# Kernel tuning notes

Hardware: AMD Instinct MI355X
Metric: run time of the kernel (lower is better)

## Reference

```python
import jax, jax.numpy as jnp
import numpy as np

# ---- hyperparameters (from init_kwargs) ----
B, SEQ, D_MODEL = 2, 2048, 1024
D_STATE, D_CONV, EXPAND, HEAD_DIM, CHUNK = 128, 4, 2, 64, 256
D_INNER = EXPAND * D_MODEL            # 2048
NH = D_INNER // HEAD_DIM              # 32 heads
CONV_DIM = D_INNER + 2 * D_STATE      # 2304
D_IN_PROJ = 2 * D_INNER + 2 * D_STATE + NH  # z, xBC, dt -> 4384
D_FF = 4 * D_MODEL
EPS = 1e-12


def setup_inputs() -> dict:
    key = jax.random.key(0)
    ks = jax.random.split(key, 16)
    s = 0.02
    f32 = jnp.float32
    inp = {
        "x": jax.random.normal(ks[0], (B, SEQ, D_MODEL), f32),
        "time_diff": jax.random.uniform(ks[1], (B, SEQ), f32),
        # TiSSD (Mamba2-style) params
        "W_in": jax.random.normal(ks[2], (D_MODEL, D_IN_PROJ), f32) * s,
        "b_in": jnp.zeros((D_IN_PROJ,), f32),
        "conv_w": jax.random.normal(ks[3], (CONV_DIM, D_CONV), f32) * s,
        "conv_b": jnp.zeros((CONV_DIM,), f32),
        "A_log": jnp.log(jnp.arange(1, NH + 1, dtype=f32)),
        "dt_bias": jnp.full((NH,), -2.0, f32),
        "D": jnp.ones((NH,), f32),
        "time_decay": jnp.full((NH,), -3.0, f32),   # time-aware decay rates
        "rms_w": jnp.ones((D_INNER,), f32),
        "W_out": jax.random.normal(ks[4], (D_INNER, D_MODEL), f32) * s,
        "b_out": jnp.zeros((D_MODEL,), f32),
        # wrapper LayerNorm
        "ln_g": jnp.ones((D_MODEL,), f32),
        "ln_b": jnp.zeros((D_MODEL,), f32),
        # FFN
        "fc1_w": jax.random.normal(ks[5], (D_MODEL, D_FF), f32) * s,
        "fc1_b": jnp.zeros((D_FF,), f32),
        "fc2_w": jax.random.normal(ks[6], (D_FF, D_MODEL), f32) * s,
        "fc2_b": jnp.zeros((D_MODEL,), f32),
        "ln2_g": jnp.ones((D_MODEL,), f32),
        "ln2_b": jnp.zeros((D_MODEL,), f32),
    }
    return inp


def _layer_norm(x, g, b, eps=EPS):
    mu = jnp.mean(x, axis=-1, keepdims=True)
    var = jnp.mean(jnp.square(x - mu), axis=-1, keepdims=True)
    return (x - mu) * jax.lax.rsqrt(var + eps) * g + b


def _hardswish(x):
    return x * jnp.clip(x + 3.0, 0.0, 6.0) * (1.0 / 6.0)


def _tissd_forward(x, time_diff, W_in, b_in, conv_w, conv_b, A_log, dt_bias, D,
                   time_decay, rms_w, W_out, b_out):
    b, l, _ = x.shape
    zxbcdt = x @ W_in + b_in                       # [b,l,D_IN_PROJ]
    z = zxbcdt[..., :D_INNER]
    xBC = zxbcdt[..., D_INNER:D_INNER + CONV_DIM]
    dt_raw = zxbcdt[..., -NH:]

    # causal depthwise conv1d (small fixed kernel -> unrolled shifts)
    xp = jnp.pad(xBC, ((0, 0), (D_CONV - 1, 0), (0, 0)))
    xBC_c = conv_b
    for k in range(D_CONV):
        xBC_c = xBC_c + xp[:, k:k + l, :] * conv_w[:, k]
    xBC_c = jax.nn.silu(xBC_c)

    xs = xBC_c[..., :D_INNER]
    Bm = xBC_c[..., D_INNER:D_INNER + D_STATE]     # [b,l,n]
    Cm = xBC_c[..., -D_STATE:]                     # [b,l,n]

    dt = jax.nn.softplus(dt_raw + dt_bias)         # [b,l,h]
    A = -jnp.exp(A_log)                            # [h]
    # time-aware: extra decay proportional to time gap
    dA = dt * A - jax.nn.softplus(time_decay) * time_diff[..., None]  # [b,l,h]

    xh = xs.reshape(b, l, NH, HEAD_DIM)
    xdt = xh * dt[..., None]                       # [b,l,h,p]

    nc = l // CHUNK
    xc = xdt.reshape(b, nc, CHUNK, NH, HEAD_DIM)
    Bc = Bm.reshape(b, nc, CHUNK, D_STATE)
    Cc = Cm.reshape(b, nc, CHUNK, D_STATE)
    dAc = dA.reshape(b, nc, CHUNK, NH).transpose(0, 3, 1, 2)  # [b,h,c,L]

    A_cum = jnp.cumsum(dAc, axis=-1)               # [b,h,c,L]
    seg = A_cum[..., :, None] - A_cum[..., None, :]
    mask = jnp.tril(jnp.ones((CHUNK, CHUNK), bool))
    Lmat = jnp.where(mask, jnp.exp(jnp.where(mask, seg, 0.0)), 0.0)  # [b,h,c,L,L]

    # intra-chunk (diagonal block) output
    Y_diag = jnp.einsum("bcln,bcsn,bhcls,bcshp->bclhp", Cc, Bc, Lmat, xc)

    # per-chunk final states
    decay_states = jnp.exp(A_cum[..., -1:] - A_cum)  # [b,h,c,L]
    states = jnp.einsum("bcln,bhcl,bclhp->bchpn", Bc, decay_states, xc)
    chunk_decay = jnp.exp(A_cum[..., -1])            # [b,h,c]

    # inter-chunk recurrence over nc chunks
    states_t = states.transpose(1, 0, 2, 3, 4)       # [c,b,h,p,n]
    decay_t = chunk_decay.transpose(2, 0, 1)         # [c,b,h]

    def step(carry, inp):
        s_c, d_c = inp
        new = carry * d_c[..., None, None] + s_c
        return new, carry                            # emit state BEFORE chunk

    init = jnp.zeros((b, NH, HEAD_DIM, D_STATE), x.dtype)
    _, prev_states = jax.lax.scan(step, init, (states_t, decay_t))
    prev_states = prev_states.transpose(1, 0, 2, 3, 4)  # [b,c,h,p,n]

    state_decay = jnp.exp(A_cum)                     # [b,h,c,L]
    Y_off = jnp.einsum("bcln,bchpn,bhcl->bclhp", Cc, prev_states, state_decay)

    Y = (Y_diag + Y_off).reshape(b, l, NH, HEAD_DIM) + D[None, None, :, None] * xh
    y = Y.reshape(b, l, D_INNER)

    # gated RMSNorm
    y = y * jax.nn.silu(z)
    y = y * jax.lax.rsqrt(jnp.mean(jnp.square(y), axis=-1, keepdims=True) + EPS) * rms_w
    return y @ W_out + b_out


def reference(x, time_diff, W_in, b_in, conv_w, conv_b, A_log, dt_bias, D,
              time_decay, rms_w, W_out, b_out, ln_g, ln_b,
              fc1_w, fc1_b, fc2_w, fc2_b, ln2_g, ln2_b):
    hidden = _tissd_forward(x, time_diff, W_in, b_in, conv_w, conv_b, A_log,
                            dt_bias, D, time_decay, rms_w, W_out, b_out)
    # num_layers > 1 -> residual; dropout is identity in eval mode
    h = _layer_norm(hidden + x, ln_g, ln_b)
    # FFN with Hardswish and residual LayerNorm
    hid = _hardswish(h @ fc1_w + fc1_b)
    hid = hid @ fc2_w + fc2_b
    out = _layer_norm(hid + h, ln2_g, ln2_b)
    return (out, time_diff)
```

## Files before the change

### kernel.cpp

```cpp
#include <hip/hip_runtime.h>

#define BATCH 2
#define SEQL 2048
#define DM 1024
#define DSTATE 128
#define HD 64
#define CHUNK 256
#define DI 2048
#define NHEADS 32
#define CONVD 2304
#define DPROJ 4384
#define DPROJ_PAD 4608
#define DFF 4096
#define NC 8
#define ROWS (BATCH*SEQL)

typedef unsigned short ushort_t;
typedef short bf16x8 __attribute__((ext_vector_type(8)));
typedef float f32x4 __attribute__((ext_vector_type(4)));

__device__ __forceinline__ float softplus_f(float v){
    return (v > 20.f) ? v : log1pf(expf(v));
}
__device__ __forceinline__ float silu_f(float v){
    return v / (1.f + expf(-v));
}
__device__ __forceinline__ ushort_t f2b(float v){
    union { float f; unsigned int u; } x; x.f = v;
    unsigned int r = x.u + 0x7fffu + ((x.u >> 16) & 1u);
    return (ushort_t)(r >> 16);
}
__device__ __forceinline__ float b2f(ushort_t v){
    union { unsigned int u; float f; } x; x.u = ((unsigned int)v) << 16;
    return x.f;
}

template<int ACT, int OUT_BF16, int TN, int NS, int DTX>
__global__ __launch_bounds__(256) void mfma_gemm_k(
    const ushort_t* __restrict__ A, const ushort_t* __restrict__ Bt,
    const float* __restrict__ bias, float* __restrict__ Cf,
    ushort_t* __restrict__ Cb, float* __restrict__ dtaux,
    int M, int N, int K, int ldc)
{
    constexpr int NT = (TN == 128) ? 4 : 2;
    constexpr int BROWS = TN / 4;
    __shared__ ushort_t As[128*64];
    __shared__ ushort_t Bs[TN*64];
    int tid = threadIdx.x;
    int lane = tid & 63, wave = tid >> 6;
    int m0 = blockIdx.y * 128, n0 = blockIdx.x * TN;
    int Ks = K / NS;
    int kb = (NS > 1) ? blockIdx.z * Ks : 0;
    int wave_m = (TN==128) ? (wave >> 1)*64 : (wave & 1)*64;
    int wave_n = (TN==128) ? (wave & 1)*64 : (wave >> 1)*32;
    int lrow = lane >> 3;
    int lcol = ((lane & 7) ^ lrow) * 8;
    const ushort_t* Abase = A  + (size_t)(m0 + wave*32    + lrow)*K + lcol + kb;
    const ushort_t* Bbase = Bt + (size_t)(n0 + wave*BROWS + lrow)*K + lcol + kb;
    ushort_t* AsW = &As[(wave*32)*64];
    ushort_t* BsW = &Bs[(wave*BROWS)*64];
    f32x4 acc[4][NT];
    #pragma unroll
    for (int i=0;i<4;i++)
        #pragma unroll
        for (int j=0;j<NT;j++) acc[i][j] = (f32x4){0.f,0.f,0.f,0.f};
    int lm = lane & 15;
    int quad = lane >> 4;
    for (int k0 = 0; k0 < Ks; k0 += 64){
        #pragma unroll
        for (int j = 0; j < 4; j++)
            __builtin_amdgcn_global_load_lds(
                (const __attribute__((address_space(1))) void*)(Abase + (size_t)(j*8)*K + k0),
                (__attribute__((address_space(3))) void*)(AsW + j*8*64), 16, 0, 0);
        #pragma unroll
        for (int j = 0; j < BROWS/8; j++)
            __builtin_amdgcn_global_load_lds(
                (const __attribute__((address_space(1))) void*)(Bbase + (size_t)(j*8)*K + k0),
                (__attribute__((address_space(3))) void*)(BsW + j*8*64), 16, 0, 0);
        __syncthreads();
        #pragma unroll
        for (int kk = 0; kk < 64; kk += 32){
            int cb = kk >> 3;
            bf16x8 af[4], bfr[NT];
            #pragma unroll
            for (int mt=0; mt<4; mt++)
                af[mt] = *(const bf16x8*)&As[(wave_m + mt*16 + lm)*64 + (((cb + quad) ^ (lm & 7))*8)];
            #pragma unroll
            for (int nt=0; nt<NT; nt++)
                bfr[nt] = *(const bf16x8*)&Bs[(wave_n + nt*16 + lm)*64 + (((cb + quad) ^ (lm & 7))*8)];
            #pragma unroll
            for (int mt=0; mt<4; mt++)
                #pragma unroll
                for (int nt=0; nt<NT; nt++)
                    acc[mt][nt] = __builtin_amdgcn_mfma_f32_16x16x32_bf16(af[mt], bfr[nt], acc[mt][nt], 0, 0, 0);
        }
        __syncthreads();
    }
    float* Cfo = Cf + (size_t)((NS > 1) ? blockIdx.z : 0) * (size_t)M * ldc;
    int addb = (NS == 1) || (blockIdx.z == 0);
    int crow0 = m0 + wave_m + quad * 4;
    int ccol0 = n0 + wave_n + lm;
    #pragma unroll
    for (int mt=0; mt<4; mt++){
        #pragma unroll
        for (int nt=0; nt<NT; nt++){
            int col = ccol0 + nt*16;
            if (col < N){
                float bv = addb ? bias[col] : 0.f;
                #pragma unroll
                for (int r=0; r<4; r++){
                    int row = crow0 + mt*16 + r;
                    float v = acc[mt][nt][r] + bv;
                    if (ACT == 1){
                        float t = fminf(fmaxf(v + 3.f, 0.f), 6.f);
                        v = v * t * (1.f/6.f);
                    }
                    if (OUT_BF16){
                        Cb[(size_t)row*ldc + col] = f2b(v);
                        if (DTX && col >= N - NHEADS)
                            dtaux[(size_t)row*NHEADS + (col - (N - NHEADS))] = v;
                    } else {
                        Cfo[(size_t)row*ldc + col] = v;
                    }
                }
            }
        }
    }
}

template<int ACT, int DTX>
__global__ __launch_bounds__(512) void gemm256_k(
    const ushort_t* __restrict__ A, const ushort_t* __restrict__ Bt,
    const float* __restrict__ bias, ushort_t* __restrict__ Cb,
    float* __restrict__ dtaux, int M, int N, int K, int ldc, int nbx)
{
    __shared__ ushort_t sm[65536];
    const int tid  = threadIdx.x;
    const int lane = tid & 63, wave = tid >> 6;
    const int lm   = lane & 15, quad = lane >> 4;
    const int wm   = wave >> 2, wn = wave & 3;
    const int nwg = gridDim.x;
    const int cpx = nwg >> 3;
    const int swz = (blockIdx.x & 7)*cpx + (blockIdx.x >> 3);
    const int bx = swz % nbx, by = swz / nbx;
    const int m0 = by << 8, n0 = bx << 8;
    const int srow = tid >> 2;
    const int scol = (((tid & 3) ^ ((srow >> 1) & 3)) << 3);
    const ushort_t* pA = A  + (size_t)(m0 + srow)*K + scol;
    const ushort_t* pB = Bt + (size_t)(n0 + srow)*K + scol;
    const size_t rstep = (size_t)128 * K;
    const int swz8 = ((quad ^ ((lm >> 1) & 3)) << 3);
    const int aoff = (wm*128 + lm)*32 + swz8;
    const int boff = 16384 + (wn*64 + lm)*32 + swz8;
    const int NT = K >> 6;

#define GL(off, src) __builtin_amdgcn_global_load_lds( \
        (const __attribute__((address_space(1))) void*)(src), \
        (__attribute__((address_space(3))) void*)(&sm[off]), 16, 0, 0)

    {
        const int d = wave*512;
        GL(d,                 pA);        GL(d + 4096,          pA + rstep);
        GL(d + 16384,         pB);        GL(d + 16384 + 4096,  pB + rstep);
        GL(d + 8192,          pA + 32);   GL(d + 8192 + 4096,   pA + 32 + rstep);
        GL(d + 24576,         pB + 32);   GL(d + 24576 + 4096,  pB + 32 + rstep);
    }
    asm volatile("s_waitcnt vmcnt(0)" ::: "memory");
    __builtin_amdgcn_sched_barrier(0);
    __builtin_amdgcn_s_barrier();

    f32x4 acc[8][4];
    #pragma unroll
    for (int i = 0; i < 8; i++)
        #pragma unroll
        for (int j = 0; j < 4; j++) acc[i][j] = (f32x4){0.f,0.f,0.f,0.f};

#define MFMA16(MH) \
    __builtin_amdgcn_s_setprio(1); \
    _Pragma("unroll") \
    for (int mt = 0; mt < 4; mt++) \
        _Pragma("unroll") \
        for (int nt = 0; nt < 4; nt++) \
            acc[(MH)*4+mt][nt] = __builtin_amdgcn_mfma_f32_16x16x32_bf16(af[mt], bf[nt], acc[(MH)*4+mt][nt], 0, 0, 0); \
    __builtin_amdgcn_s_setprio(0);

    for (int t = 0; t < NT; ++t){
        const int bo = (t & 1) << 15;
        const int nb = bo ^ 32768;
        const bool stg = (t < NT-1);
        const ushort_t* pAn = pA + (size_t)(t+1)*64;
        const ushort_t* pBn = pB + (size_t)(t+1)*64;
        bf16x8 af[4], bf[4];

        #pragma unroll
        for (int nt = 0; nt < 4; nt++) bf[nt] = *(const bf16x8*)&sm[bo + boff + nt*512];
        #pragma unroll
        for (int mt = 0; mt < 4; mt++) af[mt] = *(const bf16x8*)&sm[bo + aoff + mt*512];
        if (stg){ GL(nb + wave*512, pAn); GL(nb + 4096 + wave*512, pAn + rstep); }
        __builtin_amdgcn_s_barrier();
        asm volatile("s_waitcnt lgkmcnt(0)");
        __builtin_amdgcn_sched_barrier(0);
        MFMA16(0)
        __builtin_amdgcn_s_barrier();

        #pragma unroll
        for (int mt = 0; mt < 4; mt++) af[mt] = *(const bf16x8*)&sm[bo + aoff + 2048 + mt*512];
        if (stg){ GL(nb + 16384 + wave*512, pBn); GL(nb + 16384 + 4096 + wave*512, pBn + rstep); }
        if (stg) asm volatile("s_waitcnt vmcnt(4)" ::: "memory");
        else     asm volatile("s_waitcnt vmcnt(0)" ::: "memory");
        __builtin_amdgcn_sched_barrier(0);
        __builtin_amdgcn_s_barrier();
        asm volatile("s_waitcnt lgkmcnt(0)");
        __builtin_amdgcn_sched_barrier(0);
        MFMA16(1)
        __builtin_amdgcn_s_barrier();

        #pragma unroll
        for (int nt = 0; nt < 4; nt++) bf[nt] = *(const bf16x8*)&sm[bo + 8192 + boff + nt*512];
        #pragma unroll
        for (int mt = 0; mt < 4; mt++) af[mt] = *(const bf16x8*)&sm[bo + 8192 + aoff + 2048 + mt*512];
        if (stg){ GL(nb + 8192 + wave*512, pAn + 32); GL(nb + 8192 + 4096 + wave*512, pAn + 32 + rstep); }
        __builtin_amdgcn_s_barrier();
        asm volatile("s_waitcnt lgkmcnt(0)");
        __builtin_amdgcn_sched_barrier(0);
        MFMA16(1)
        __builtin_amdgcn_s_barrier();

        #pragma unroll
        for (int mt = 0; mt < 4; mt++) af[mt] = *(const bf16x8*)&sm[bo + 8192 + aoff + mt*512];
        if (stg){
            GL(nb + 24576 + wave*512, pBn + 32); GL(nb + 24576 + 4096 + wave*512, pBn + 32 + rstep);
            asm volatile("s_waitcnt vmcnt(4)" ::: "memory");
            __builtin_amdgcn_sched_barrier(0);
        }
        __builtin_amdgcn_s_barrier();
        asm volatile("s_waitcnt lgkmcnt(0)");
        __builtin_amdgcn_sched_barrier(0);
        MFMA16(0)
        __builtin_amdgcn_s_barrier();
    }
#undef MFMA16
#undef GL

    const int crow = m0 + wm*128 + quad*4;
    const int ccol = n0 + wn*64 + lm;
    #pragma unroll
    for (int m8 = 0; m8 < 8; m8++){
        #pragma unroll
        for (int nt = 0; nt < 4; nt++){
            int col = ccol + nt*16;
            if (col < N){
                float bv = bias[col];
                #pragma unroll
                for (int r = 0; r < 4; r++){
                    int row = crow + m8*16 + r;
                    float v = acc[m8][nt][r] + bv;
                    if (ACT == 1){
                        float tt = fminf(fmaxf(v + 3.f, 0.f), 6.f);
                        v = v * tt * (1.f/6.f);
                    }
                    Cb[(size_t)row*ldc + col] = f2b(v);
                    if (DTX && col >= N - NHEADS)
                        dtaux[(size_t)row*NHEADS + (col - (N - NHEADS))] = v;
                }
            }
        }
    }
}

__global__ __launch_bounds__(256) void prep_in_k(const float* __restrict__ x,
                                                 ushort_t* __restrict__ x_bf,
                                                 const float* __restrict__ W_in,
                                                 ushort_t* __restrict__ WinT){
    __shared__ ushort_t tile[32][33];
    int bid = blockIdx.x;
    if (bid < 16384){
        int idx = bid*256 + threadIdx.x;
        x_bf[idx] = f2b(x[idx]);
        return;
    }
    int id2 = bid - 16384;
    int n0 = (id2 % 144)*32, k0 = (id2 / 144)*32;
    int tx = threadIdx.x & 31, ty = threadIdx.x >> 5;
    #pragma unroll
    for (int i = 0; i < 4; i++){
        int k = k0 + ty + i*8;
        int n = n0 + tx;
        float v = (n < DPROJ) ? W_in[(size_t)k*DPROJ + n] : 0.f;
        tile[ty + i*8][tx] = f2b(v);
    }
    __syncthreads();
    #pragma unroll
    for (int i = 0; i < 4; i++)
        WinT[(size_t)(n0 + ty + i*8)*DM + k0 + tx] = tile[tx][ty + i*8];
}

__global__ __launch_bounds__(256) void transpose3_k(const float* __restrict__ Wout,
                                                    const float* __restrict__ fc1w,
                                                    const float* __restrict__ fc2w,
                                                    ushort_t* __restrict__ WoutT,
                                                    ushort_t* __restrict__ fc1T,
                                                    ushort_t* __restrict__ fc2T){
    __shared__ ushort_t tile[32][33];
    int bid = blockIdx.x;
    const float* W; ushort_t* Wt; int K, N, gx, id;
    if (bid < 2048){        W = Wout; Wt = WoutT; K = DI;  N = DM;  gx = 32;  id = bid; }
    else if (bid < 6144){   W = fc1w; Wt = fc1T;  K = DM;  N = DFF; gx = 128; id = bid - 2048; }
    else {                  W = fc2w; Wt = fc2T;  K = DFF; N = DM;  gx = 32;  id = bid - 6144; }
    int n0 = (id % gx)*32, k0 = (id / gx)*32;
    int tx = threadIdx.x & 31, ty = threadIdx.x >> 5;
    #pragma unroll
    for (int i = 0; i < 4; i++){
        int k = k0 + ty + i*8;
        int n = n0 + tx;
        tile[ty + i*8][tx] = f2b(W[(size_t)k*N + n]);
    }
    __syncthreads();
    #pragma unroll
    for (int i = 0; i < 4; i++)
        Wt[(size_t)(n0 + ty + i*8)*K + k0 + tx] = tile[tx][ty + i*8];
}

#define CONVBLKS (ROWS*CONVD/256)
__global__ __launch_bounds__(256) void conv_dt_k(const ushort_t* __restrict__ zx,
                                                 const float* __restrict__ conv_w,
                                                 const float* __restrict__ conv_b,
                                                 ushort_t* __restrict__ convb,
                                                 const float* __restrict__ dtaux,
                                                 const float* __restrict__ time_diff,
                                                 const float* __restrict__ A_log,
                                                 const float* __restrict__ dt_bias,
                                                 const float* __restrict__ time_decay,
                                                 float* __restrict__ dtH,
                                                 float* __restrict__ Acum){
    __shared__ float s[CHUNK];
    int bid = blockIdx.x;
    if (bid < CONVBLKS){
        int idx = bid*256 + threadIdx.x;
        int c = idx % CONVD;
        int row = idx / CONVD;
        int t = row & (SEQL-1);
        float acc = conv_b[c];
        #pragma unroll
        for (int k = 0; k < 4; k++){
            int tt = t + k - 3;
            if (tt >= 0)
                acc += b2f(zx[((size_t)(row + k - 3))*DPROJ + DI + c]) * conv_w[c*4 + k];
        }
        convb[idx] = f2b(silu_f(acc));
        return;
    }
    int id2 = bid - CONVBLKS;
    int c = id2 % NC;
    int h = (id2 / NC) % NHEADS;
    int b = id2 / (NC*NHEADS);
    int l = threadIdx.x;
    int t = c*CHUNK + l;
    float dtr = dtaux[((size_t)(b*SEQL + t))*NHEADS + h];
    float dtv = softplus_f(dtr + dt_bias[h]);
    float A = -expf(A_log[h]);
    float dA = dtv*A - softplus_f(time_decay[h]) * time_diff[b*SEQL + t];
    dtH[((size_t)(b*NHEADS + h))*SEQL + t] = dtv;
    s[l] = dA;
    __syncthreads();
    for (int off = 1; off < CHUNK; off <<= 1){
        float v = (l >= off) ? s[l-off] : 0.f;
        __syncthreads();
        s[l] += v;
        __syncthreads();
    }
    Acum[((size_t)(b*NHEADS + h))*SEQL + t] = s[l];
}

__global__ __launch_bounds__(256) void g_mfma_k(const ushort_t* __restrict__ convb,
                                                ushort_t* __restrict__ G){
    __shared__ ushort_t As[64*136];
    __shared__ ushort_t Bs[64*136];
    int bc = blockIdx.z;
    int l0 = blockIdx.y*64, s0 = blockIdx.x*64;
    int tid = threadIdx.x;
    int lane = tid & 63, wave = tid >> 6;
    int lm = lane & 15, quad = lane >> 4;
    const ushort_t* base = convb + (size_t)bc*CHUNK*CONVD;
    #pragma unroll
    for (int i = 0; i < 4; i++){
        int e = tid + i*256;
        int r = e >> 4, k = (e & 15)*8;
        *(bf16x8*)&As[r*136 + k] = *(const bf16x8*)&base[(size_t)(l0+r)*CONVD + DI + DSTATE + k];
        *(bf16x8*)&Bs[r*136 + k] = *(const bf16x8*)&base[(size_t)(s0+r)*CONVD + DI + k];
    }
    __syncthreads();
    f32x4 acc[4];
    #pragma unroll
    for (int j=0;j<4;j++) acc[j] = (f32x4){0.f,0.f,0.f,0.f};
    #pragma unroll
    for (int kk = 0; kk < 4; kk++){
        bf16x8 af = *(const bf16x8*)&As[(wave*16+lm)*136 + kk*32 + quad*8];
        #pragma unroll
        for (int nt = 0; nt < 4; nt++){
            bf16x8 bfr = *(const bf16x8*)&Bs[(nt*16+lm)*136 + kk*32 + quad*8];
            acc[nt] = __builtin_amdgcn_mfma_f32_16x16x32_bf16(af, bfr, acc[nt], 0, 0, 0);
        }
    }
    ushort_t* g = G + (size_t)bc*CHUNK*CHUNK;
    #pragma unroll
    for (int nt = 0; nt < 4; nt++)
        #pragma unroll
        for (int r = 0; r < 4; r++)
            g[(size_t)(l0 + wave*16 + quad*4 + r)*CHUNK + s0 + nt*16 + lm] = f2b(acc[nt][r]);
}

#define RSX 264
#define RSB 72
__global__ __launch_bounds__(256) void states_mfma_k(const ushort_t* __restrict__ convb,
                                                     const float* __restrict__ dtH,
                                                     const float* __restrict__ Acum,
                                                     float* __restrict__ states){
    __shared__ ushort_t xw[64*RSX];
    __shared__ ushort_t Bt[128*RSB];
    __shared__ float Acs[CHUNK];
    __shared__ float dts[CHUNK];
    int bid = blockIdx.x;
    int h = bid % NHEADS;
    int c = (bid / NHEADS) % NC;
    int b = bid / (NHEADS*NC);
    int tid = threadIdx.x;
    int lane = tid & 63, wave = tid >> 6;
    int lm = lane & 15, quad = lane >> 4;
    Acs[tid] = Acum[((size_t)(b*NHEADS + h))*SEQL + c*CHUNK + tid];
    dts[tid] = dtH[((size_t)(b*NHEADS + h))*SEQL + c*CHUNK + tid];
    __syncthreads();
    float AcL = Acs[CHUNK-1];
    {
        const ushort_t* xg = convb + ((size_t)(b*SEQL + c*CHUNK))*CONVD + h*HD;
        #pragma unroll
        for (int j8 = 0; j8 < 8; j8++){
            int s0 = wave*64 + j8*8;
            bf16x8 pk;
            #pragma unroll
            for (int j = 0; j < 8; j++){
                int l = s0 + j;
                pk[j] = (short)f2b(expf(AcL - Acs[l]) * dts[l] * b2f(xg[(size_t)l*CONVD + lane]));
            }
            *(bf16x8*)&xw[lane*RSX + s0] = pk;
        }
    }
    f32x4 acc[8];
    #pragma unroll
    for (int j=0;j<8;j++) acc[j] = (f32x4){0.f,0.f,0.f,0.f};
    const ushort_t* bbase = convb + ((size_t)(b*SEQL + c*CHUNK))*CONVD + DI;
    for (int l0 = 0; l0 < CHUNK; l0 += 64){
        __syncthreads();
        #pragma unroll
        for (int i = 0; i < 32; i++){
            int e = tid + i*256; int l = e >> 7, n = e & 127;
            Bt[n*RSB + l] = bbase[(size_t)(l0+l)*CONVD + n];
        }
        __syncthreads();
        #pragma unroll
        for (int kk = 0; kk < 2; kk++){
            bf16x8 af = *(const bf16x8*)&xw[(wave*16+lm)*RSX + l0 + kk*32 + quad*8];
            #pragma unroll
            for (int nt = 0; nt < 8; nt++){
                bf16x8 bfr = *(const bf16x8*)&Bt[(nt*16+lm)*RSB + kk*32 + quad*8];
                acc[nt] = __builtin_amdgcn_mfma_f32_16x16x32_bf16(af, bfr, acc[nt], 0, 0, 0);
            }
        }
    }
    float* outp = states + ((size_t)((b*NC + c)*NHEADS + h))*(HD*DSTATE);
    #pragma unroll
    for (int nt = 0; nt < 8; nt++)
        #pragma unroll
        for (int r = 0; r < 4; r++)
            outp[(size_t)(wave*16 + quad*4 + r)*DSTATE + nt*16 + lm] = acc[nt][r];
}

__global__ __launch_bounds__(256) void prev_scan_k(const float* __restrict__ states,
                                                   const float* __restrict__ Acum,
                                                   float* __restrict__ prev){
    int bid = blockIdx.x;
    int part = bid & 15;
    int h = (bid >> 4) & (NHEADS-1);
    int b = bid >> 9;
    int tid = threadIdx.x;
    const float* AcB = Acum + ((size_t)(b*NHEADS + h))*SEQL;
    float dec[NC];
    #pragma unroll
    for (int c = 0; c < NC; c++) dec[c] = expf(AcB[c*CHUNK + CHUNK-1]);
    #pragma unroll
    for (int j = 0; j < 2; j++){
        int e = part*512 + j*256 + tid;
        float carry = 0.f;
        #pragma unroll
        for (int c = 0; c < NC; c++){
            size_t idx = ((size_t)((b*NC + c)*NHEADS + h))*(HD*DSTATE) + e;
            prev[idx] = carry;
            carry = carry*dec[c] + states[idx];
        }
    }
}

#define RLX 264
#define RLP 136
__global__ __launch_bounds__(256) void y_mfma_k(const ushort_t* __restrict__ convb,
                                                const ushort_t* __restrict__ G,
                                                const float* __restrict__ Acum,
                                                const float* __restrict__ dtH,
                                                const float* __restrict__ prev,
                                                const float* __restrict__ Dp,
                                                ushort_t* __restrict__ Ybf){
    __shared__ ushort_t xdtT[64*RLX];
    __shared__ ushort_t prevs[64*RLP];
    __shared__ float Acs[CHUNK];
    __shared__ float dts[CHUNK];
    int bid = blockIdx.x;
    int h = bid % NHEADS;
    int c = (bid / NHEADS) % NC;
    int b = bid / (NHEADS*NC);
    int tid = threadIdx.x;
    int lane = tid & 63, wave = tid >> 6;
    int lm = lane & 15, quad = lane >> 4;

    Acs[tid] = Acum[((size_t)(b*NHEADS + h))*SEQL + c*CHUNK + tid];
    dts[tid] = dtH[((size_t)(b*NHEADS + h))*SEQL + c*CHUNK + tid];
    {
        const float* pv = prev + ((size_t)((b*NC + c)*NHEADS + h))*(HD*DSTATE);
        #pragma unroll
        for (int i = 0; i < 32; i++){
            int e = tid + i*256; int p = e >> 7, n = e & 127;
            prevs[p*RLP + n] = f2b(pv[e]);
        }
    }
    __syncthreads();
    {
        const ushort_t* xg = convb + ((size_t)(b*SEQL + c*CHUNK))*CONVD + h*HD;
        #pragma unroll
        for (int j8 = 0; j8 < 8; j8++){
            int s0 = wave*64 + j8*8;
            bf16x8 pk;
            #pragma unroll
            for (int j = 0; j < 8; j++){
                int l = s0 + j;
                pk[j] = (short)f2b(b2f(xg[(size_t)l*CONVD + lane]) * dts[l]);
            }
            *(bf16x8*)&xdtT[lane*RLX + s0] = pk;
        }
    }
    __syncthreads();

    int   lrow[4];  float Alr[4], eAlr[4];
    #pragma unroll
    for (int mt = 0; mt < 4; mt++){
        lrow[mt] = (mt*4 + wave)*16 + lm;
        Alr[mt]  = Acs[lrow[mt]];
        eAlr[mt] = expf(Alr[mt]);
    }
    const ushort_t* Gbase = G + ((size_t)(b*NC + c))*(CHUNK*CHUNK);

    f32x4 acc[4][4];
    #pragma unroll
    for (int i=0;i<4;i++)
        #pragma unroll
        for (int j=0;j<4;j++) acc[i][j] = (f32x4){0.f,0.f,0.f,0.f};

    for (int ks = 0; ks < 8; ks++){
        bf16x8 bfr[4];
        #pragma unroll
        for (int nt = 0; nt < 4; nt++)
            bfr[nt] = *(const bf16x8*)&xdtT[(nt*16+lm)*RLX + ks*32 + quad*8];
        #pragma unroll
        for (int mt = 0; mt < 4; mt++){
            int rblk = mt*4 + wave;
            int nst = rblk/2 + 1;
            if (ks < nst){
                int sbase = ks*32 + quad*8;
                bf16x8 g8 = *(const bf16x8*)&Gbase[(size_t)lrow[mt]*CHUNK + sbase];
                const float4* A4 = (const float4*)(&Acs[sbase]);
                float4 a0 = A4[0], a1 = A4[1];
                float Al = Alr[mt]; int l = lrow[mt];
                float pv[8];
                pv[0] = (sbase+0 <= l) ? b2f((ushort_t)g8[0])*expf(Al - a0.x) : 0.f;
                pv[1] = (sbase+1 <= l) ? b2f((ushort_t)g8[1])*expf(Al - a0.y) : 0.f;
                pv[2] = (sbase+2 <= l) ? b2f((ushort_t)g8[2])*expf(Al - a0.z) : 0.f;
                pv[3] = (sbase+3 <= l) ? b2f((ushort_t)g8[3])*expf(Al - a0.w) : 0.f;
                pv[4] = (sbase+4 <= l) ? b2f((ushort_t)g8[4])*expf(Al - a1.x) : 0.f;
                pv[5] = (sbase+5 <= l) ? b2f((ushort_t)g8[5])*expf(Al - a1.y) : 0.f;
                pv[6] = (sbase+6 <= l) ? b2f((ushort_t)g8[6])*expf(Al - a1.z) : 0.f;
                pv[7] = (sbase+7 <= l) ? b2f((ushort_t)g8[7])*expf(Al - a1.w) : 0.f;
                bf16x8 af;
                #pragma unroll
                for (int j = 0; j < 8; j++) af[j] = (short)f2b(pv[j]);
                #pragma unroll
                for (int nt = 0; nt < 4; nt++)
                    acc[mt][nt] = __builtin_amdgcn_mfma_f32_16x16x32_bf16(af, bfr[nt], acc[mt][nt], 0, 0, 0);
            }
        }
    }
    for (int kc = 0; kc < 4; kc++){
        bf16x8 bfr[4];
        #pragma unroll
        for (int nt = 0; nt < 4; nt++)
            bfr[nt] = *(const bf16x8*)&prevs[(nt*16+lm)*RLP + kc*32 + quad*8];
        #pragma unroll
        for (int mt = 0; mt < 4; mt++){
            int rowg = b*SEQL + c*CHUNK + lrow[mt];
            bf16x8 c8 = *(const bf16x8*)&convb[(size_t)rowg*CONVD + DI + DSTATE + kc*32 + quad*8];
            float e = eAlr[mt];
            bf16x8 af;
            #pragma unroll
            for (int j = 0; j < 8; j++) af[j] = (short)f2b(e * b2f((ushort_t)c8[j]));
            #pragma unroll
            for (int nt = 0; nt < 4; nt++)
                acc[mt][nt] = __builtin_amdgcn_mfma_f32_16x16x32_bf16(af, bfr[nt], acc[mt][nt], 0, 0, 0);
        }
    }
    float Dv = Dp[h];
    #pragma unroll
    for (int mt = 0; mt < 4; mt++){
        int l0 = (mt*4 + wave)*16 + quad*4;
        #pragma unroll
        for (int nt = 0; nt < 4; nt++){
            int p = nt*16 + lm;
            #pragma unroll
            for (int r = 0; r < 4; r++){
                int rowg = b*SEQL + c*CHUNK + l0 + r;
                float xs = b2f(convb[(size_t)rowg*CONVD + h*HD + p]);
                Ybf[(size_t)rowg*DI + h*HD + p] = f2b(acc[mt][nt][r] + Dv*xs);
            }
        }
    }
}

__global__ __launch_bounds__(256) void gate_rms_k(const ushort_t* __restrict__ Yb,
                                                  const ushort_t* __restrict__ zx,
                                                  const float* __restrict__ rms_w,
                                                  ushort_t* __restrict__ yn){
    __shared__ float red[4];
    __shared__ float scale_s;
    int row = blockIdx.x; int tid = threadIdx.x;
    float v[8]; float ss = 0.f;
    #pragma unroll
    for (int i = 0; i < 8; i++){
        int d = tid + i*256;
        float g = b2f(Yb[(size_t)row*DI + d]) * silu_f(b2f(zx[(size_t)row*DPROJ + d]));
        v[i] = g; ss += g*g;
    }
    #pragma unroll
    for (int off = 32; off > 0; off >>= 1) ss += __shfl_down(ss, off);
    int lane = tid & 63, wid = tid >> 6;
    if (lane == 0) red[wid] = ss;
    __syncthreads();
    if (tid == 0) scale_s = rsqrtf((red[0]+red[1]+red[2]+red[3])*(1.f/DI) + 1e-12f);
    __syncthreads();
    float sc = scale_s;
    #pragma unroll
    for (int i = 0; i < 8; i++){
        int d = tid + i*256;
        yn[(size_t)row*DI + d] = f2b(v[i]*sc*rms_w[d]);
    }
}

__global__ __launch_bounds__(256) void ln_hbf_k(const float* __restrict__ a,
                                                const float* __restrict__ a2,
                                                const float* __restrict__ resid,
                                                const float* __restrict__ g,
                                                const float* __restrict__ bw,
                                                ushort_t* __restrict__ bfout){
    __shared__ float redA[4], redB[4];
    __shared__ float mu_s, rs_s;
    int row = blockIdx.x; int tid = threadIdx.x;
    float u[4]; float s = 0.f, s2 = 0.f;
    #pragma unroll
    for (int i = 0; i < 4; i++){
        int d = tid + i*256;
        float val = a[(size_t)row*DM + d] + a2[(size_t)row*DM + d] + resid[(size_t)row*DM + d];
        u[i] = val; s += val; s2 += val*val;
    }
    #pragma unroll
    for (int off = 32; off > 0; off >>= 1){
        s  += __shfl_down(s,  off);
        s2 += __shfl_down(s2, off);
    }
    int lane = tid & 63, wid = tid >> 6;
    if (lane == 0){ redA[wid] = s; redB[wid] = s2; }
    __syncthreads();
    if (tid == 0){
        float S  = redA[0]+redA[1]+redA[2]+redA[3];
        float S2 = redB[0]+redB[1]+redB[2]+redB[3];
        float mu = S*(1.f/DM);
        float var = S2*(1.f/DM) - mu*mu;
        mu_s = mu; rs_s = rsqrtf(var + 1e-12f);
    }
    __syncthreads();
    float mu = mu_s, rs = rs_s;
    #pragma unroll
    for (int i = 0; i < 4; i++){
        int d = tid + i*256;
        bfout[(size_t)row*DM + d] = f2b((u[i]-mu)*rs*g[d] + bw[d]);
    }
}

__global__ __launch_bounds__(256) void ln_final_k(const float* __restrict__ a,
                                                  const float* __restrict__ a2,
                                                  const ushort_t* __restrict__ residb,
                                                  const float* __restrict__ g,
                                                  const float* __restrict__ bw,
                                                  float* __restrict__ outp,
                                                  const float* __restrict__ td){
    __shared__ float redA[4], redB[4];
    __shared__ float mu_s, rs_s;
    int row = blockIdx.x; int tid = threadIdx.x;
    if (row >= ROWS){
        int idx = (row - ROWS)*256 + tid;
        outp[(size_t)ROWS*DM + idx] = td[idx];
        return;
    }
    float u[4]; float s = 0.f, s2 = 0.f;
    #pragma unroll
    for (int i = 0; i < 4; i++){
        int d = tid + i*256;
        float val = a[(size_t)row*DM + d] + a2[(size_t)row*DM + d] + b2f(residb[(size_t)row*DM + d]);
        u[i] = val; s += val; s2 += val*val;
    }
    #pragma unroll
    for (int off = 32; off > 0; off >>= 1){
        s  += __shfl_down(s,  off);
        s2 += __shfl_down(s2, off);
    }
    int lane = tid & 63, wid = tid >> 6;
    if (lane == 0){ redA[wid] = s; redB[wid] = s2; }
    __syncthreads();
    if (tid == 0){
        float S  = redA[0]+redA[1]+redA[2]+redA[3];
        float S2 = redB[0]+redB[1]+redB[2]+redB[3];
        float mu = S*(1.f/DM);
        float var = S2*(1.f/DM) - mu*mu;
        mu_s = mu; rs_s = rsqrtf(var + 1e-12f);
    }
    __syncthreads();
    float mu = mu_s, rs = rs_s;
    #pragma unroll
    for (int i = 0; i < 4; i++){
        int d = tid + i*256;
        outp[(size_t)row*DM + d] = (u[i]-mu)*rs*g[d] + bw[d];
    }
}

extern "C" void kernel_launch(void* const* d_in, const int* in_sizes, int n_in,
                              void* d_out, int out_size, void* d_ws, size_t ws_size,
                              hipStream_t stream){
    const float* x         = (const float*)d_in[0];
    const float* time_diff = (const float*)d_in[1];
    const float* W_in      = (const float*)d_in[2];
    const float* b_in      = (const float*)d_in[3];
    const float* conv_w    = (const float*)d_in[4];
    const float* conv_b    = (const float*)d_in[5];
    const float* A_log     = (const float*)d_in[6];
    const float* dt_bias   = (const float*)d_in[7];
    const float* Dp        = (const float*)d_in[8];
    const float* time_dec  = (const float*)d_in[9];
    const float* rms_w     = (const float*)d_in[10];
    const float* W_out     = (const float*)d_in[11];
    const float* b_out     = (const float*)d_in[12];
    const float* ln_g      = (const float*)d_in[13];
    const float* ln_b      = (const float*)d_in[14];
    const float* fc1_w     = (const float*)d_in[15];
    const float* fc1_b     = (const float*)d_in[16];
    const float* fc2_w     = (const float*)d_in[17];
    const float* fc2_b     = (const float*)d_in[18];
    const float* ln2_g     = (const float*)d_in[19];
    const float* ln2_b     = (const float*)d_in[20];

    float* ws = (float*)d_ws;
    float* zx    = ws;
    float* convb = zx    + 17956864;
    float* dtH   = convb + 9437184;
    float* Acum  = dtH   + 131072;
    float* r4    = Acum  + 131072;
    float* r5    = r4    + 8388608;
    float* ybreg = r5    + 9437184;
    ushort_t* zx_bf  = (ushort_t*)zx;
    float*    dtaux  = zx + 10600000;
    ushort_t* mid_bf = (ushort_t*)zx;
    ushort_t* h_bf   = (ushort_t*)(zx + 8388608);
    ushort_t* convb_bf = (ushort_t*)convb;
    float* outPa  = convb;
    ushort_t* x_bf  = (ushort_t*)r4;
    ushort_t* WinT  = (ushort_t*)(r4 + 2097152);
    ushort_t* WoutT = (ushort_t*)(r4 + 4194304);
    float* fc2Pa = r4;
    ushort_t* Gb   = (ushort_t*)r5;
    float* stat = r5 + 1048576;
    float* prev = stat + 4194304;
    ushort_t* yn_bf = (ushort_t*)r5;
    ushort_t* fc1T  = (ushort_t*)(r5 + 4194304);
    ushort_t* fc2T  = (ushort_t*)(r5 + 6291456);
    ushort_t* Ybf = (ushort_t*)ybreg;
    float* outp   = (float*)d_out;

    prep_in_k<<<16384 + 4608, 256, 0, stream>>>(x, x_bf, W_in, WinT);
    gemm256_k<0,1><<<288, 512, 0, stream>>>(x_bf, WinT, b_in, zx_bf, dtaux, ROWS, DPROJ, DM, DPROJ, 18);
    conv_dt_k<<<CONVBLKS + BATCH*NHEADS*NC, 256, 0, stream>>>(zx_bf, conv_w, conv_b, convb_bf,
                                                              dtaux, time_diff, A_log, dt_bias, time_dec, dtH, Acum);
    g_mfma_k<<<dim3(4,4,BATCH*NC), 256, 0, stream>>>(convb_bf, Gb);
    states_mfma_k<<<BATCH*NC*NHEADS, 256, 0, stream>>>(convb_bf, dtH, Acum, stat);
    prev_scan_k<<<BATCH*NHEADS*16, 256, 0, stream>>>(stat, Acum, prev);
    y_mfma_k<<<BATCH*NC*NHEADS, 256, 0, stream>>>(convb_bf, Gb, Acum, dtH, prev, Dp, Ybf);
    gate_rms_k<<<ROWS, 256, 0, stream>>>(Ybf, zx_bf, rms_w, yn_bf);
    transpose3_k<<<10240, 256, 0, stream>>>(W_out, fc1_w, fc2_w, WoutT, fc1T, fc2T);
    mfma_gemm_k<0,0,64,2,0><<<dim3(DM/64, ROWS/128, 2), 256, 0, stream>>>(yn_bf, WoutT, b_out, outPa, nullptr, nullptr, ROWS, DM, DI, DM);
    ln_hbf_k<<<ROWS, 256, 0, stream>>>(outPa, outPa + (size_t)ROWS*DM, x, ln_g, ln_b, h_bf);
    gemm256_k<1,0><<<256, 512, 0, stream>>>(h_bf, fc1T, fc1_b, mid_bf, nullptr, ROWS, DFF, DM, DFF, 16);
    mfma_gemm_k<0,0,64,2,0><<<dim3(DM/64, ROWS/128, 2), 256, 0, stream>>>(mid_bf, fc2T, fc2_b, fc2Pa, nullptr, nullptr, ROWS, DM, DFF, DM);
    ln_final_k<<<ROWS + ROWS/256, 256, 0, stream>>>(fc2Pa, fc2Pa + (size_t)ROWS*DM, h_bf, ln2_g, ln2_b, outp, time_diff);
}
```

Measured before the change: 480.4 us.

## Use 256-tile GEMM with 4-way split-K for output and FC2 projections

The W_out and fc2 projections move from the 128-row mfma_gemm with 2-way split-K to the 256x256-tile gemm256 kernel with 4-way split-K. The four fp32 partials are summed in the following LayerNorm kernels, which now take four partial inputs. The input projection is split: the 32 dt columns go to a small mfma_gemm launch that writes the fp32 dt auxiliary output, and gemm256 handles the first 4352 columns with 272 blocks. The aim is better tile reuse and CU occupancy for the N=1024 GEMMs, at the cost of more partial-sum memory traffic and an extra launch.

```diff
diff --git a/kernel.cpp b/kernel.cpp
--- a/kernel.cpp
+++ b/kernel.cpp
@@ -128,11 +128,13 @@
     }
 }
 
-template<int ACT, int DTX>
+template<int ACT, int OUTF, int NSPL>
 __global__ __launch_bounds__(512) void gemm256_k(
     const ushort_t* __restrict__ A, const ushort_t* __restrict__ Bt,
     const float* __restrict__ bias, ushort_t* __restrict__ Cb,
-    float* __restrict__ dtaux, int M, int N, int K, int ldc, int nbx)
+    float* __restrict__ f0, float* __restrict__ f1,
+    float* __restrict__ f2, float* __restrict__ f3,
+    int M, int N, int K, int ldc, int nbx)
 {
     __shared__ ushort_t sm[65536];
     const int tid  = threadIdx.x;
@@ -144,15 +146,17 @@
     const int swz = (blockIdx.x & 7)*cpx + (blockIdx.x >> 3);
     const int bx = swz % nbx, by = swz / nbx;
     const int m0 = by << 8, n0 = bx << 8;
+    const int ksp = (NSPL > 1) ? blockIdx.y : 0;
+    const int Kpb = K / NSPL;
+    const int NT  = Kpb >> 6;
     const int srow = tid >> 2;
     const int scol = (((tid & 3) ^ ((srow >> 1) & 3)) << 3);
-    const ushort_t* pA = A  + (size_t)(m0 + srow)*K + scol;
-    const ushort_t* pB = Bt + (size_t)(n0 + srow)*K + scol;
+    const ushort_t* pA = A  + (size_t)(m0 + srow)*K + scol + (size_t)ksp*Kpb;
+    const ushort_t* pB = Bt + (size_t)(n0 + srow)*K + scol + (size_t)ksp*Kpb;
     const size_t rstep = (size_t)128 * K;
     const int swz8 = ((quad ^ ((lm >> 1) & 3)) << 3);
     const int aoff = (wm*128 + lm)*32 + swz8;
     const int boff = 16384 + (wn*64 + lm)*32 + swz8;
-    const int NT = K >> 6;
 
 #define GL(off, src) __builtin_amdgcn_global_load_lds( \
         (const __attribute__((address_space(1))) void*)(src), \
@@ -244,13 +248,14 @@
 
     const int crow = m0 + wm*128 + quad*4;
     const int ccol = n0 + wn*64 + lm;
+    float* fo = (NSPL > 1) ? ((ksp==0)?f0:(ksp==1)?f1:(ksp==2)?f2:f3) : f0;
     #pragma unroll
     for (int m8 = 0; m8 < 8; m8++){
         #pragma unroll
         for (int nt = 0; nt < 4; nt++){
             int col = ccol + nt*16;
             if (col < N){
-                float bv = bias[col];
+                float bv = (ksp == 0) ? bias[col] : 0.f;
                 #pragma unroll
                 for (int r = 0; r < 4; r++){
                     int row = crow + m8*16 + r;
@@ -259,9 +264,8 @@
                         float tt = fminf(fmaxf(v + 3.f, 0.f), 6.f);
                         v = v * tt * (1.f/6.f);
                     }
-                    Cb[(size_t)row*ldc + col] = f2b(v);
-                    if (DTX && col >= N - NHEADS)
-                        dtaux[(size_t)row*NHEADS + (col - (N - NHEADS))] = v;
+                    if (OUTF) fo[(size_t)row*ldc + col] = v;
+                    else      Cb[(size_t)row*ldc + col] = f2b(v);
                 }
             }
         }
@@ -660,8 +664,10 @@
     }
 }
 
-__global__ __launch_bounds__(256) void ln_hbf_k(const float* __restrict__ a,
+__global__ __launch_bounds__(256) void ln_hbf_k(const float* __restrict__ a0,
+                                                const float* __restrict__ a1,
                                                 const float* __restrict__ a2,
+                                                const float* __restrict__ a3,
                                                 const float* __restrict__ resid,
                                                 const float* __restrict__ g,
                                                 const float* __restrict__ bw,
@@ -673,7 +679,8 @@
     #pragma unroll
     for (int i = 0; i < 4; i++){
         int d = tid + i*256;
-        float val = a[(size_t)row*DM + d] + a2[(size_t)row*DM + d] + resid[(size_t)row*DM + d];
+        size_t ix = (size_t)row*DM + d;
+        float val = a0[ix] + a1[ix] + a2[ix] + a3[ix] + resid[ix];
         u[i] = val; s += val; s2 += val*val;
     }
     #pragma unroll
@@ -700,8 +707,10 @@
     }
 }
 
-__global__ __launch_bounds__(256) void ln_final_k(const float* __restrict__ a,
+__global__ __launch_bounds__(256) void ln_final_k(const float* __restrict__ a0,
+                                                  const float* __restrict__ a1,
                                                   const float* __restrict__ a2,
+                                                  const float* __restrict__ a3,
                                                   const ushort_t* __restrict__ residb,
                                                   const float* __restrict__ g,
                                                   const float* __restrict__ bw,
@@ -719,7 +728,8 @@
     #pragma unroll
     for (int i = 0; i < 4; i++){
         int d = tid + i*256;
-        float val = a[(size_t)row*DM + d] + a2[(size_t)row*DM + d] + b2f(residb[(size_t)row*DM + d]);
+        size_t ix = (size_t)row*DM + d;
+        float val = a0[ix] + a1[ix] + a2[ix] + a3[ix] + b2f(residb[ix]);
         u[i] = val; s += val; s2 += val*val;
     }
     #pragma unroll
@@ -784,11 +794,9 @@
     ushort_t* mid_bf = (ushort_t*)zx;
     ushort_t* h_bf   = (ushort_t*)(zx + 8388608);
     ushort_t* convb_bf = (ushort_t*)convb;
-    float* outPa  = convb;
     ushort_t* x_bf  = (ushort_t*)r4;
     ushort_t* WinT  = (ushort_t*)(r4 + 2097152);
     ushort_t* WoutT = (ushort_t*)(r4 + 4194304);
-    float* fc2Pa = r4;
     ushort_t* Gb   = (ushort_t*)r5;
     float* stat = r5 + 1048576;
     float* prev = stat + 4194304;
@@ -796,10 +804,22 @@
     ushort_t* fc1T  = (ushort_t*)(r5 + 4194304);
     ushort_t* fc2T  = (ushort_t*)(r5 + 6291456);
     ushort_t* Ybf = (ushort_t*)ybreg;
+    float* oP0 = convb;
+    float* oP1 = convb + 4194304;
+    float* oP2 = ybreg;
+    float* oP3 = r4;
+    float* fP0 = r4;
+    float* fP1 = r4 + 4194304;
+    float* fP2 = r5;
+    float* fP3 = ybreg;
     float* outp   = (float*)d_out;
 
     prep_in_k<<<16384 + 4608, 256, 0, stream>>>(x, x_bf, W_in, WinT);
-    gemm256_k<0,1><<<288, 512, 0, stream>>>(x_bf, WinT, b_in, zx_bf, dtaux, ROWS, DPROJ, DM, DPROJ, 18);
+    mfma_gemm_k<0,1,64,1,1><<<dim3(1, ROWS/128), 256, 0, stream>>>(
+        x_bf, WinT + (size_t)4352*DM, b_in + 4352, nullptr,
+        zx_bf + 4352, dtaux, ROWS, 32, DM, DPROJ);
+    gemm256_k<0,0,1><<<272, 512, 0, stream>>>(x_bf, WinT, b_in, zx_bf,
+        nullptr, nullptr, nullptr, nullptr, ROWS, DPROJ, DM, DPROJ, 17);
     conv_dt_k<<<CONVBLKS + BATCH*NHEADS*NC, 256, 0, stream>>>(zx_bf, conv_w, conv_b, convb_bf,
                                                               dtaux, time_diff, A_log, dt_bias, time_dec, dtH, Acum);
     g_mfma_k<<<dim3(4,4,BATCH*NC), 256, 0, stream>>>(convb_bf, Gb);
@@ -808,9 +828,12 @@
     y_mfma_k<<<BATCH*NC*NHEADS, 256, 0, stream>>>(convb_bf, Gb, Acum, dtH, prev, Dp, Ybf);
     gate_rms_k<<<ROWS, 256, 0, stream>>>(Ybf, zx_bf, rms_w, yn_bf);
     transpose3_k<<<10240, 256, 0, stream>>>(W_out, fc1_w, fc2_w, WoutT, fc1T, fc2T);
-    mfma_gemm_k<0,0,64,2,0><<<dim3(DM/64, ROWS/128, 2), 256, 0, stream>>>(yn_bf, WoutT, b_out, outPa, nullptr, nullptr, ROWS, DM, DI, DM);
-    ln_hbf_k<<<ROWS, 256, 0, stream>>>(outPa, outPa + (size_t)ROWS*DM, x, ln_g, ln_b, h_bf);
-    gemm256_k<1,0><<<256, 512, 0, stream>>>(h_bf, fc1T, fc1_b, mid_bf, nullptr, ROWS, DFF, DM, DFF, 16);
-    mfma_gemm_k<0,0,64,2,0><<<dim3(DM/64, ROWS/128, 2), 256, 0, stream>>>(mid_bf, fc2T, fc2_b, fc2Pa, nullptr, nullptr, ROWS, DM, DFF, DM);
-    ln_final_k<<<ROWS + ROWS/256, 256, 0, stream>>>(fc2Pa, fc2Pa + (size_t)ROWS*DM, h_bf, ln2_g, ln2_b, outp, time_diff);
-}
+    gemm256_k<0,1,4><<<dim3(64, 4), 512, 0, stream>>>(yn_bf, WoutT, b_out, nullptr,
+        oP0, oP1, oP2, oP3, ROWS, DM, DI, DM, 4);
+    ln_hbf_k<<<ROWS, 256, 0, stream>>>(oP0, oP1, oP2, oP3, x, ln_g, ln_b, h_bf);
+    gemm256_k<1,0,1><<<256, 512, 0, stream>>>(h_bf, fc1T, fc1_b, mid_bf,
+        nullptr, nullptr, nullptr, nullptr, ROWS, DFF, DM, DFF, 16);
+    gemm256_k<0,1,4><<<dim3(64, 4), 512, 0, stream>>>(mid_bf, fc2T, fc2_b, nullptr,
+        fP0, fP1, fP2, fP3, ROWS, DM, DFF, DM, 4);
+    ln_final_k<<<ROWS + ROWS/256, 256, 0, stream>>>(fP0, fP1, fP2, fP3, h_bf, ln2_g, ln2_b, outp, time_diff);
+}
```

After: 507.2 us. +5.6%, slower.
